# Optimization experiments

Hardware: AMD Instinct MI355X
Metric: run time of the kernel (lower is better)

The kernel has to match this reference:

```python
import jax, jax.numpy as jnp
import numpy as np

DIM = 96
HID = 384
DEPTH = 5
HEADS = 8
INNER = 64 * DIM          # inner_dim = dim_head * dim per source (dim_head=64)
DH = INNER // HEADS       # per-head dim = 768
SCALE = 64 ** -0.5        # scale uses default dim_head=64, not actual per-head dim
EPS = 1e-5


def setup_inputs() -> dict:
    key = jax.random.key(0)
    ks = jax.random.split(key, 13)
    def p(k, shape, s=0.02):
        return jax.random.normal(k, shape, jnp.float32) * s
    return {
        "x": jax.random.normal(ks[0], (2, 512, DIM), jnp.float32),
        "gam_a": p(ks[1], (DEPTH, 3, DIM)),          # attention pre-norm gammas
        "Wq": p(ks[2], (DEPTH, 3, DIM, INNER)),
        "Wk": p(ks[3], (DEPTH, 3, DIM, INNER)),
        "Wv": p(ks[4], (DEPTH, 3, DIM, INNER)),
        "Wo": p(ks[5], (DEPTH, 3, INNER, DIM)),
        "gam_m": p(ks[6], (DEPTH, 2, DIM)),          # MLP pre-norm gammas
        "W1": p(ks[7], (DEPTH, 2, DIM, HID)),
        "b1": p(ks[8], (DEPTH, 2, HID)),
        "W2": p(ks[9], (DEPTH, 2, HID, DIM)),
        "b2": p(ks[10], (DEPTH, 2, DIM)),
        "gam_mid": p(ks[11], (DEPTH, DIM)),          # bare LayerNorm inside each block
        "gam_final": p(ks[12], (DIM,)),
    }


def _ln(x, g):
    # nn.LayerNorm(elementwise_affine=False) followed by x * (gamma + 1)
    mu = x.mean(-1, keepdims=True)
    var = ((x - mu) ** 2).mean(-1, keepdims=True)
    return (x - mu) * jax.lax.rsqrt(var + EPS) * (g + 1.0)


def _attn(x, g, wq, wk, wv, wo):
    b, n, _ = x.shape
    h = _ln(x, g)                                    # self.norm (reuse_attention=True)
    q = (h @ wq).reshape(b, n, HEADS, DH).transpose(0, 2, 1, 3) * SCALE
    k = (h @ wk).reshape(b, n, HEADS, DH).transpose(0, 2, 1, 3)
    v = (h @ wv).reshape(b, n, HEADS, DH).transpose(0, 2, 1, 3)
    sim = jnp.einsum("bhid,bhjd->bhij", q, k)        # [b,h,n,n]
    a = jax.nn.softmax(sim, axis=-1)                 # dropout=0.0 -> identity
    o = jnp.einsum("bhij,bhjd->bhid", a, v)
    return o.transpose(0, 2, 1, 3).reshape(b, n, INNER) @ wo


def _mlp(x, g, w1, b1_, w2, b2_):
    # LayerNorm -> Linear -> GELU(exact) -> Linear (dropouts eval-mode identity)
    h = jax.nn.gelu(_ln(x, g) @ w1 + b1_, approximate=False)
    return h @ w2 + b2_


def reference(x, gam_a, Wq, Wk, Wv, Wo, gam_m, W1, b1, W2, b2, gam_mid, gam_final):
    for d in range(DEPTH):
        x = _attn(x, gam_a[d, 0], Wq[d, 0], Wk[d, 0], Wv[d, 0], Wo[d, 0]) + x
        x = _mlp(x, gam_m[d, 0], W1[d, 0], b1[d, 0], W2[d, 0], b2[d, 0]) + x
        x = _attn(x, gam_a[d, 1], Wq[d, 1], Wk[d, 1], Wv[d, 1], Wo[d, 1]) + x
        x = _attn(x, gam_a[d, 2], Wq[d, 2], Wk[d, 2], Wv[d, 2], Wo[d, 2]) + x
        x = _ln(x, gam_mid[d])                       # bare LayerNorm, NO residual
        x = _mlp(x, gam_m[d, 1], W1[d, 1], b1[d, 1], W2[d, 1], b2[d, 1]) + x
    return _ln(x, gam_final)
```

## Files before the change

### kernel.cpp

```cpp
#include <hip/hip_runtime.h>
#include <hip/hip_bf16.h>

typedef __hip_bfloat16 bf16;
typedef __attribute__((ext_vector_type(8))) short bf16x8;
typedef __attribute__((ext_vector_type(4))) float f32x4;

#define TOK    1024
#define DIM    96
#define HIDN   384
#define HEADS  8
#define DH     768
#define INNER  6144
#define SEQ    512
#define NDEPTH 5
#define EPSLN  1e-5f
#define QSCALE 0.125f

#define MFMA16(a, b, c) __builtin_amdgcn_mfma_f32_16x16x32_bf16((a), (b), (c), 0, 0, 0)

__device__ __forceinline__ float b2f(bf16 v) { return __bfloat162float(v); }
__device__ __forceinline__ bf16  f2b(float v) { return __float2bfloat16(v); }

__device__ __forceinline__ float gload(const void* p, size_t i, int f) {
  return f ? b2f(((const bf16*)p)[i]) : ((const float*)p)[i];
}
__device__ __forceinline__ const char* gptr(const void* base, size_t off, int f) {
  return (const char*)base + off * (size_t)(f ? 2 : 4);
}

__device__ __forceinline__ uint4 pack8(float4 u0, float4 u1) {
  alignas(16) unsigned short o[8];
  bf16 t;
  t = f2b(u0.x); o[0] = *(unsigned short*)&t;
  t = f2b(u0.y); o[1] = *(unsigned short*)&t;
  t = f2b(u0.z); o[2] = *(unsigned short*)&t;
  t = f2b(u0.w); o[3] = *(unsigned short*)&t;
  t = f2b(u1.x); o[4] = *(unsigned short*)&t;
  t = f2b(u1.y); o[5] = *(unsigned short*)&t;
  t = f2b(u1.z); o[6] = *(unsigned short*)&t;
  t = f2b(u1.w); o[7] = *(unsigned short*)&t;
  return *(const uint4*)o;
}

__global__ __launch_bounds__(256) void detect_kernel(const void* xraw, int* flag) {
  __shared__ int cnt[256];
  int t = threadIdx.x;
  const unsigned short* u = (const unsigned short*)xraw;
  int c = 0;
  #pragma unroll
  for (int i = 0; i < 4; i++) {
    unsigned short h = u[2 * (t * 4 + i)];
    int e = (h >> 7) & 0xFF;
    if (e >= 87 && e <= 132) c++;
  }
  cnt[t] = c;
  __syncthreads();
  for (int s = 128; s > 0; s >>= 1) {
    if (t < s) cnt[t] += cnt[t + s];
    __syncthreads();
  }
  if (t == 0) *flag = (cnt[0] > 700) ? 1 : 0;
}

__global__ __launch_bounds__(256) void wtrans_all_kernel(
    const void* __restrict__ Wo, const void* __restrict__ W1,
    const void* __restrict__ W2, bf16* __restrict__ woT,
    bf16* __restrict__ w1T, bf16* __restrict__ w2T,
    const int* __restrict__ flagp) {
  __shared__ float tile[32][65];
  int f = *flagp;
  int b = blockIdx.x;
  const void* src; bf16* dst; int R, C, bx, by, bz;
  if (b < 5760) {
    src = Wo; dst = woT; R = INNER; C = DIM;
    bz = b / 384; int rem = b % 384; bx = rem & 1; by = rem >> 1;
  } else if (b < 5940) {
    int idx = b - 5760;
    src = W1; dst = w1T; R = DIM; C = HIDN;
    bx = idx % 6; by = (idx / 6) % 3; bz = idx / 18;
  } else {
    int idx = b - 5940;
    src = W2; dst = w2T; R = HIDN; C = DIM;
    bx = idx & 1; by = (idx >> 1) % 12; bz = idx / 24;
  }
  int t = threadIdx.x;
  int c0 = bx * 64, r0 = by * 32;
  size_t bb = (size_t)bz * R * C;
  int ty = t >> 4, tx = t & 15;
  #pragma unroll
  for (int half = 0; half < 2; half++) {
    int r = r0 + ty + half * 16;
    int c = c0 + tx * 4;
    if (c < C) {
      size_t idx = bb + (size_t)r * C + c;
      float v0, v1, v2, v3;
      if (f) {
        uint2 u = *(const uint2*)((const unsigned short*)src + idx);
        v0 = __uint_as_float((u.x & 0xffffu) << 16);
        v1 = __uint_as_float(u.x & 0xffff0000u);
        v2 = __uint_as_float((u.y & 0xffffu) << 16);
        v3 = __uint_as_float(u.y & 0xffff0000u);
      } else {
        float4 v = *(const float4*)((const float*)src + idx);
        v0 = v.x; v1 = v.y; v2 = v.z; v3 = v.w;
      }
      tile[ty + half * 16][tx * 4 + 0] = v0;
      tile[ty + half * 16][tx * 4 + 1] = v1;
      tile[ty + half * 16][tx * 4 + 2] = v2;
      tile[ty + half * 16][tx * 4 + 3] = v3;
    }
  }
  __syncthreads();
  int cc = c0 + (t >> 2), rseg = (t & 3) * 8;
  if (cc < C) {
    int cs = cc - c0;
    alignas(16) unsigned short o[8];
    #pragma unroll
    for (int j = 0; j < 8; j++) {
      bf16 tv = f2b(tile[rseg + j][cs]);
      o[j] = *(unsigned short*)&tv;
    }
    *(uint4*)&dst[bb + (size_t)cc * R + r0 + rseg] = *(const uint4*)o;
  }
}

template <int WM>
__device__ __forceinline__ void gemm_bt_body(
    const void* __restrict__ A, int aF32, int lda,
    const void* __restrict__ Bt, int bF32, int ldb,
    int m0, int n0, int kbeg, int kend, int Mtot, int N,
    float alpha, bf16* __restrict__ Cb, float* __restrict__ Cf, int ldc) {
  constexpr int TM = WM * 32;
  __shared__ bf16 As[TM][40];
  __shared__ bf16 Bs[128][40];
  int t = threadIdx.x;
  int lane = t & 63;
  int wave = t >> 6;
  int wm = (wave >> 1) * (WM * 16), wn = (wave & 1) * 64;
  f32x4 acc[WM][4];
  #pragma unroll
  for (int i = 0; i < WM; i++)
    #pragma unroll
    for (int j = 0; j < 4; j++) acc[i][j] = (f32x4){0.f, 0.f, 0.f, 0.f};

  int arow = t >> 2, aseg = (t & 3) * 8;

  for (int kb = kbeg; kb < kend; kb += 32) {
    #pragma unroll
    for (int i = 0; i < (TM + 63) / 64; i++) {
      int rr = arow + i * 64;
      if ((TM % 64 == 0) || rr < TM) {
        int gm = min(m0 + rr, Mtot - 1);
        size_t idx = (size_t)gm * lda + kb + aseg;
        if (aF32) {
          const float* Af = (const float*)A;
          float4 u0 = *(const float4*)(Af + idx);
          float4 u1 = *(const float4*)(Af + idx + 4);
          *(uint4*)&As[rr][aseg] = pack8(u0, u1);
        } else {
          *(uint4*)&As[rr][aseg] = *(const uint4*)((const bf16*)A + idx);
        }
      }
    }
    #pragma unroll
    for (int i = 0; i < 2; i++) {
      int r = arow + i * 64;
      int gn = n0 + r;
      if (gn < N) {
        size_t idx = (size_t)gn * ldb + kb + aseg;
        if (bF32) {
          const float* Bf = (const float*)Bt;
          float4 u0 = *(const float4*)(Bf + idx);
          float4 u1 = *(const float4*)(Bf + idx + 4);
          *(uint4*)&Bs[r][aseg] = pack8(u0, u1);
        } else {
          *(uint4*)&Bs[r][aseg] = *(const uint4*)((const bf16*)Bt + idx);
        }
      } else {
        uint4 zz = {0, 0, 0, 0};
        *(uint4*)&Bs[r][aseg] = zz;
      }
    }
    __syncthreads();
    int fm = lane & 15, fq = (lane >> 4) * 8;
    bf16x8 af[WM], bfv[4];
    #pragma unroll
    for (int i = 0; i < WM; i++)
      af[i] = *(const bf16x8*)&As[wm + i * 16 + fm][fq];
    #pragma unroll
    for (int j = 0; j < 4; j++)
      bfv[j] = *(const bf16x8*)&Bs[wn + j * 16 + fm][fq];
    #pragma unroll
    for (int i = 0; i < WM; i++)
      #pragma unroll
      for (int j = 0; j < 4; j++)
        acc[i][j] = MFMA16(af[i], bfv[j], acc[i][j]);
    __syncthreads();
  }
  int col = lane & 15, rq = (lane >> 4) * 4;
  #pragma unroll
  for (int j = 0; j < 4; j++) {
    int gn = n0 + wn + j * 16 + col;
    if (gn >= N) continue;
    #pragma unroll
    for (int i = 0; i < WM; i++) {
      #pragma unroll
      for (int r = 0; r < 4; r++) {
        int gm = m0 + wm + i * 16 + rq + r;
        if (gm >= Mtot) continue;
        if (Cf) Cf[(size_t)gm * ldc + gn] = acc[i][j][r];
        else    Cb[(size_t)gm * ldc + gn] = f2b(acc[i][j][r] * alpha);
      }
    }
  }
}

__global__ __launch_bounds__(256) void mtgt_kernel(
    const void* __restrict__ WqE, const void* __restrict__ WkE,
    const void* __restrict__ WvE, const bf16* __restrict__ woT,
    float* __restrict__ P, const int* __restrict__ flagp) {
  int f = *flagp;
  int z = blockIdx.z;
  int ks = blockIdx.x / 3, mt = blockIdx.x % 3;
  bool isM = z < 120;
  int zz = isM ? z : z - 120;
  int L = zz >> 3, h = zz & 7;
  size_t wo = (size_t)L * DIM * INNER + (size_t)h * DH;
  const void* A  = isM ? (const void*)((const char*)WkE + wo * (f ? 2 : 4))
                       : (const void*)(woT + wo);
  const void* Bt = isM ? (const void*)((const char*)WqE + wo * (f ? 2 : 4))
                       : (const void*)((const char*)WvE + wo * (f ? 2 : 4));
  int aF32 = isM ? !f : 0;
  int bF32 = !f;
  float* Cf = P + ((size_t)ks * 240 + z) * DIM * DIM;
  gemm_bt_body<1>(A, aF32, INNER, Bt, bF32, INNER,
                  mt * 32, 0, ks * (DH / 2), (ks + 1) * (DH / 2), DIM, DIM,
                  1.f, nullptr, Cf, DIM);
}

__device__ __forceinline__ void ln_row_vals(float v0, float v1in, int lane,
    const char* g, int f, float& o0, float& o1) {
  float v1 = (lane < 32) ? v1in : 0.f;
  float s = v0 + v1;
  #pragma unroll
  for (int off = 32; off > 0; off >>= 1) s += __shfl_xor(s, off);
  float mu = s * (1.f / 96.f);
  float d0 = v0 - mu;
  float d1 = (lane < 32) ? (v1 - mu) : 0.f;
  float q = d0 * d0 + d1 * d1;
  #pragma unroll
  for (int off = 32; off > 0; off >>= 1) q += __shfl_xor(q, off);
  float rstd = rsqrtf(q * (1.f / 96.f) + EPSLN);
  o0 = d0 * rstd * (gload(g, lane, f) + 1.f);
  o1 = (lane < 32) ? (d1 * rstd * (gload(g, 64 + lane, f) + 1.f)) : 0.f;
}

__device__ __forceinline__ void store_hn(bf16* hn, bf16* hnT, int row, int lane,
                                         float o0, float o1) {
  size_t base = (size_t)row * DIM;
  bf16* hT = hnT + (size_t)(row >> 9) * DIM * SEQ;
  int ss = row & (SEQ - 1);
  hn[base + lane] = f2b(o0);
  hT[(size_t)lane * SEQ + ss] = f2b(o0);
  if (lane < 32) {
    hn[base + 64 + lane] = f2b(o1);
    hT[(size_t)(64 + lane) * SEQ + ss] = f2b(o1);
  }
}

__global__ __launch_bounds__(256) void cvtcast_kernel(
    const float* __restrict__ P, bf16* __restrict__ Mt, bf16* __restrict__ Gt,
    const void* __restrict__ in_x, float* __restrict__ x,
    bf16* __restrict__ hn, bf16* __restrict__ hnT,
    const void* __restrict__ gb, const int* __restrict__ flagp) {
  if (blockIdx.x < 2160) {
    const int n = 240 * DIM * DIM;
    int i0 = (blockIdx.x * 256 + threadIdx.x) * 4;
    if (i0 >= n) return;
    int z = i0 / (DIM * DIM);
    bool isM = z < 120;
    float alpha = isM ? QSCALE : 1.f;
    float4 a = *(const float4*)(P + i0);
    float4 b = *(const float4*)(P + n + i0);
    bf16* out = isM ? (Mt + i0) : (Gt + (size_t)i0 - (size_t)120 * DIM * DIM);
    alignas(8) unsigned short o[4];
    bf16 t;
    t = f2b((a.x + b.x) * alpha); o[0] = *(unsigned short*)&t;
    t = f2b((a.y + b.y) * alpha); o[1] = *(unsigned short*)&t;
    t = f2b((a.z + b.z) * alpha); o[2] = *(unsigned short*)&t;
    t = f2b((a.w + b.w) * alpha); o[3] = *(unsigned short*)&t;
    *(uint2*)out = *(const uint2*)o;
  } else {
    int f = *flagp;
    int wave = threadIdx.x >> 6, lane = threadIdx.x & 63;
    int row = (blockIdx.x - 2160) * 4 + wave;
    size_t base = (size_t)row * DIM;
    float v0 = gload(in_x, base + lane, f);
    float v1 = (lane < 32) ? gload(in_x, base + 64 + lane, f) : 0.f;
    x[base + lane] = v0;
    if (lane < 32) x[base + 64 + lane] = v1;
    float o0, o1;
    ln_row_vals(v0, v1, lane, gptr(gb, 0, f), f, o0, o1);
    store_hn(hn, hnT, row, lane, o0, o1);
  }
}

__global__ __launch_bounds__(256) void ln_kernel(
    const float* __restrict__ x, bf16* __restrict__ hn, bf16* __restrict__ hnT,
    const void* __restrict__ gb, size_t goff, const int* __restrict__ flagp) {
  int f = *flagp;
  int wave = threadIdx.x >> 6, lane = threadIdx.x & 63;
  int row = blockIdx.x * 4 + wave;
  size_t base = (size_t)row * DIM;
  float v0 = x[base + lane];
  float v1 = (lane < 32) ? x[base + 64 + lane] : 0.f;
  float o0, o1;
  ln_row_vals(v0, v1, lane, gptr(gb, goff, f), f, o0, o1);
  store_hn(hn, hnT, row, lane, o0, o1);
}

__global__ __launch_bounds__(512) void fattn5_kernel(
    const bf16* __restrict__ hn,
    const bf16* __restrict__ hnT,
    const bf16* __restrict__ MtL,
    const bf16* __restrict__ GtL,
    float* __restrict__ x) {
  __shared__ bf16 tP[16][520];
  __shared__ bf16 Zs[16][104];
  __shared__ float red[2][8][16];
  int tid = threadIdx.x, lane = tid & 63, wave = tid >> 6;
  int fm = lane & 15, fq = (lane >> 4) * 8;
  int col = lane & 15, rq = (lane >> 4) * 4;
  int z = blockIdx.y, b = z >> 3, h = z & 7;
  int m0 = blockIdx.x * 16;
  const bf16* hnB = hn + (size_t)b * SEQ * DIM;
  const bf16* hTB = hnT + (size_t)b * DIM * SEQ;
  const bf16* MtH = MtL + (size_t)h * DIM * DIM;
  const bf16* GtH = GtL + (size_t)h * DIM * DIM;

  if (wave < 6) {
    int n = wave;
    f32x4 a0 = (f32x4){0.f, 0.f, 0.f, 0.f};
    #pragma unroll
    for (int kb = 0; kb < 96; kb += 32) {
      bf16x8 af = *(const bf16x8*)(hnB + (size_t)(m0 + fm) * DIM + kb + fq);
      bf16x8 bv = *(const bf16x8*)(MtH + (size_t)(n * 16 + fm) * DIM + kb + fq);
      a0 = MFMA16(af, bv, a0);
    }
    #pragma unroll
    for (int r = 0; r < 4; r++)
      Zs[rq + r][n * 16 + col] = f2b(a0[r]);
  }
  __syncthreads();

  f32x4 acc2[4];
  #pragma unroll
  for (int j = 0; j < 4; j++) acc2[j] = (f32x4){0.f, 0.f, 0.f, 0.f};
  #pragma unroll
  for (int kb = 0; kb < 96; kb += 32) {
    bf16x8 af = *(const bf16x8*)&Zs[fm][kb + fq];
    bf16x8 bv[4];
    #pragma unroll
    for (int j = 0; j < 4; j++)
      bv[j] = *(const bf16x8*)(hnB + (size_t)(wave * 64 + j * 16 + fm) * DIM + kb + fq);
    #pragma unroll
    for (int j = 0; j < 4; j++)
      acc2[j] = MFMA16(af, bv[j], acc2[j]);
  }

  float rmax[4];
  #pragma unroll
  for (int r = 0; r < 4; r++) {
    float m = -1e30f;
    #pragma unroll
    for (int j = 0; j < 4; j++) m = fmaxf(m, acc2[j][r]);
    rmax[r] = m;
  }
  #pragma unroll
  for (int s = 1; s < 16; s <<= 1)
    #pragma unroll
    for (int r = 0; r < 4; r++)
      rmax[r] = fmaxf(rmax[r], __shfl_xor(rmax[r], s));
  if (col == 0)
    #pragma unroll
    for (int r = 0; r < 4; r++) red[0][wave][rq + r] = rmax[r];
  __syncthreads();
  float rsum[4];
  #pragma unroll
  for (int r = 0; r < 4; r++) {
    int row = rq + r;
    float gm = red[0][0][row];
    #pragma unroll
    for (int q = 1; q < 8; q++) gm = fmaxf(gm, red[0][q][row]);
    float s = 0.f;
    #pragma unroll
    for (int j = 0; j < 4; j++) {
      float e = __expf(acc2[j][r] - gm);
      acc2[j][r] = e;
      s += e;
    }
    rsum[r] = s;
  }
  #pragma unroll
  for (int s = 1; s < 16; s <<= 1)
    #pragma unroll
    for (int r = 0; r < 4; r++)
      rsum[r] += __shfl_xor(rsum[r], s);
  if (col == 0)
    #pragma unroll
    for (int r = 0; r < 4; r++) red[1][wave][rq + r] = rsum[r];
  __syncthreads();

  #pragma unroll
  for (int r = 0; r < 4; r++) {
    int row = rq + r;
    float tot = red[1][0][row];
    #pragma unroll
    for (int q = 1; q < 8; q++) tot += red[1][q][row];
    float inv = 1.f / tot;
    #pragma unroll
    for (int j = 0; j < 4; j++)
      tP[row][wave * 64 + j * 16 + col] = f2b(acc2[j][r] * inv);
  }
  __syncthreads();

  if (wave < 6) {
    int n = wave;
    f32x4 z0 = (f32x4){0.f, 0.f, 0.f, 0.f};
    #pragma unroll 4
    for (int kb = 0; kb < 512; kb += 32) {
      bf16x8 bv = *(const bf16x8*)(hTB + (size_t)(n * 16 + fm) * SEQ + kb + fq);
      bf16x8 af = *(const bf16x8*)&tP[fm][kb + fq];
      z0 = MFMA16(af, bv, z0);
    }
    __syncthreads();
    #pragma unroll
    for (int r = 0; r < 4; r++)
      Zs[rq + r][n * 16 + col] = f2b(z0[r]);
  } else {
    __syncthreads();
  }
  __syncthreads();

  if (wave < 6) {
    int n = wave;
    f32x4 o0 = (f32x4){0.f, 0.f, 0.f, 0.f};
    #pragma unroll
    for (int kb = 0; kb < 96; kb += 32) {
      bf16x8 af = *(const bf16x8*)&Zs[fm][kb + fq];
      bf16x8 bv = *(const bf16x8*)(GtH + (size_t)(n * 16 + fm) * DIM + kb + fq);
      o0 = MFMA16(af, bv, o0);
    }
    #pragma unroll
    for (int r = 0; r < 4; r++) {
      int gr = b * SEQ + m0 + rq + r;
      atomicAdd(x + (size_t)gr * DIM + n * 16 + col, o0[r]);
    }
  }
}

__global__ __launch_bounds__(512) void fmlp_kernel(
    float* __restrict__ X,
    const void* __restrict__ gmidb, size_t gmidoff, int useMid,
    const void* __restrict__ gmb, size_t gmoff,
    const bf16* __restrict__ w1T,
    const void* __restrict__ b1b, size_t b1off,
    const bf16* __restrict__ w2T,
    const void* __restrict__ b2b, size_t b2off,
    int lnmode, const void* __restrict__ lngb, size_t lngoff,
    bf16* __restrict__ hn, bf16* __restrict__ hnT, void* __restrict__ dout,
    const int* __restrict__ flagp) {
  __shared__ float X1s[32][96];
  __shared__ bf16 As[32][104];
  __shared__ bf16 Hs[32][392];
  int f = *flagp;
  int tid = threadIdx.x, lane = tid & 63, wave = tid >> 6;
  int fm = lane & 15, fq = (lane >> 4) * 8;
  int col = lane & 15, rq = (lane >> 4) * 4;
  int m0 = blockIdx.x * 32;
  const char* gm = gptr(gmb, gmoff, f);
  float gm0 = gload(gm, lane, f) + 1.f;
  float gm1 = (lane < 32) ? (gload(gm, 64 + lane, f) + 1.f) : 0.f;
  float gd0 = 1.f, gd1 = 1.f;
  if (useMid) {
    const char* gmid = gptr(gmidb, gmidoff, f);
    gd0 = gload(gmid, lane, f) + 1.f;
    gd1 = (lane < 32) ? (gload(gmid, 64 + lane, f) + 1.f) : 0.f;
  }
  for (int r = wave; r < 32; r += 8) {
    const float* xr = X + (size_t)(m0 + r) * DIM;
    float v0 = xr[lane];
    float v1 = (lane < 32) ? xr[64 + lane] : 0.f;
    if (useMid) {
      float s = v0 + v1;
      #pragma unroll
      for (int off = 32; off > 0; off >>= 1) s += __shfl_xor(s, off);
      float mu = s * (1.f / 96.f);
      float d0 = v0 - mu;
      float d1 = (lane < 32) ? (v1 - mu) : 0.f;
      float q = d0 * d0 + d1 * d1;
      #pragma unroll
      for (int off = 32; off > 0; off >>= 1) q += __shfl_xor(q, off);
      float rstd = rsqrtf(q * (1.f / 96.f) + EPSLN);
      v0 = d0 * rstd * gd0;
      v1 = (lane < 32) ? (d1 * rstd * gd1) : 0.f;
    }
    X1s[r][lane] = v0;
    if (lane < 32) X1s[r][64 + lane] = v1;
    float s = v0 + v1;
    #pragma unroll
    for (int off = 32; off > 0; off >>= 1) s += __shfl_xor(s, off);
    float mu = s * (1.f / 96.f);
    float d0 = v0 - mu;
    float d1 = (lane < 32) ? (v1 - mu) : 0.f;
    float q = d0 * d0 + d1 * d1;
    #pragma unroll
    for (int off = 32; off > 0; off >>= 1) q += __shfl_xor(q, off);
    float rstd = rsqrtf(q * (1.f / 96.f) + EPSLN);
    As[r][lane] = f2b(d0 * rstd * gm0);
    if (lane < 32) As[r][64 + lane] = f2b(d1 * rstd * gm1);
  }
  __syncthreads();

  int mw = wave & 1, nh = wave >> 1;
  f32x4 acc1[6];
  #pragma unroll
  for (int j = 0; j < 6; j++) acc1[j] = (f32x4){0.f, 0.f, 0.f, 0.f};
  #pragma unroll
  for (int kb = 0; kb < 96; kb += 32) {
    bf16x8 af = *(const bf16x8*)&As[mw * 16 + fm][kb + fq];
    #pragma unroll
    for (int j = 0; j < 6; j++) {
      bf16x8 bv = *(const bf16x8*)(w1T + (size_t)(nh * 96 + j * 16 + fm) * DIM + kb + fq);
      acc1[j] = MFMA16(af, bv, acc1[j]);
    }
  }
  const char* b1p = gptr(b1b, b1off, f);
  #pragma unroll
  for (int j = 0; j < 6; j++) {
    int gn = nh * 96 + j * 16 + col;
    float bv = gload(b1p, gn, f);
    #pragma unroll
    for (int r = 0; r < 4; r++) {
      float v = acc1[j][r] + bv;
      v = 0.5f * v * (1.f + erff(v * 0.70710678118f));
      Hs[mw * 16 + rq + r][gn] = f2b(v);
    }
  }
  __syncthreads();

  if (wave < 6) {
    int mA = wave & 1, nb = wave >> 1;
    f32x4 o0 = (f32x4){0.f, 0.f, 0.f, 0.f}, o1 = o0;
    #pragma unroll 4
    for (int kb = 0; kb < 384; kb += 32) {
      bf16x8 af = *(const bf16x8*)&Hs[mA * 16 + fm][kb + fq];
      bf16x8 b0 = *(const bf16x8*)(w2T + (size_t)(nb * 16 + fm) * HIDN + kb + fq);
      bf16x8 b1 = *(const bf16x8*)(w2T + (size_t)((nb + 3) * 16 + fm) * HIDN + kb + fq);
      o0 = MFMA16(af, b0, o0);
      o1 = MFMA16(af, b1, o1);
    }
    const char* b2p = gptr(b2b, b2off, f);
    float bb0 = gload(b2p, nb * 16 + col, f);
    float bb1 = gload(b2p, (nb + 3) * 16 + col, f);
    #pragma unroll
    for (int r = 0; r < 4; r++) {
      int row = mA * 16 + rq + r;
      int gmr = m0 + row;
      float nv0 = X1s[row][nb * 16 + col] + o0[r] + bb0;
      float nv1 = X1s[row][(nb + 3) * 16 + col] + o1[r] + bb1;
      X[(size_t)gmr * DIM + nb * 16 + col] = nv0;
      X[(size_t)gmr * DIM + (nb + 3) * 16 + col] = nv1;
      X1s[row][nb * 16 + col] = nv0;
      X1s[row][(nb + 3) * 16 + col] = nv1;
    }
  }
  __syncthreads();

  const char* lg = gptr(lngb, lngoff, f);
  for (int r = wave; r < 32; r += 8) {
    int row = m0 + r;
    size_t base = (size_t)row * DIM;
    float v0 = X1s[r][lane];
    float v1 = (lane < 32) ? X1s[r][64 + lane] : 0.f;
    float o0, o1;
    ln_row_vals(v0, v1, lane, lg, f, o0, o1);
    if (lnmode == 1) {
      store_hn(hn, hnT, row, lane, o0, o1);
    } else {
      if (!f) {
        ((float*)dout)[base + lane] = o0;
        if (lane < 32) ((float*)dout)[base + 64 + lane] = o1;
      } else {
        ((bf16*)dout)[base + lane] = f2b(o0);
        if (lane < 32) ((bf16*)dout)[base + 64 + lane] = f2b(o1);
      }
    }
  }
}

extern "C" void kernel_launch(void* const* d_in, const int* in_sizes, int n_in,
                              void* d_out, int out_size, void* d_ws, size_t ws_size,
                              hipStream_t stream) {
  const void* in_x    = d_in[0];
  const void* gam_a   = d_in[1];
  const void* Wq      = d_in[2];
  const void* Wk      = d_in[3];
  const void* Wv      = d_in[4];
  const void* Wo      = d_in[5];
  const void* gam_m   = d_in[6];
  const void* W1      = d_in[7];
  const void* b1      = d_in[8];
  const void* W2      = d_in[9];
  const void* b2      = d_in[10];
  const void* gam_mid = d_in[11];
  const void* gam_fin = d_in[12];

  char* wsb = (char*)d_ws;
  size_t off = 0;
  auto carve = [&](size_t bytes) {
    char* p = wsb + off;
    off += (bytes + 255) & ~(size_t)255;
    return p;
  };
  int*   flag = (int*)carve(256);
  float* x    = (float*)carve((size_t)TOK * DIM * 4);
  bf16*  hn   = (bf16*)carve((size_t)TOK * DIM * 2);
  bf16*  hnT  = (bf16*)carve((size_t)2 * DIM * SEQ * 2);
  const size_t WSZ = (size_t)15 * DIM * INNER;
  bf16*  woT  = (bf16*)carve(WSZ * 2);
  bf16*  w1T  = (bf16*)carve((size_t)10 * DIM * HIDN * 2);
  bf16*  w2T  = (bf16*)carve((size_t)10 * DIM * HIDN * 2);
  bf16*  Mt   = (bf16*)carve((size_t)120 * DIM * DIM * 2);
  bf16*  Gt   = (bf16*)carve((size_t)120 * DIM * DIM * 2);
  float* MtP  = (float*)carve((size_t)2 * 240 * DIM * DIM * 4);

  detect_kernel<<<dim3(1), dim3(256), 0, stream>>>(in_x, flag);

  wtrans_all_kernel<<<dim3(6180), dim3(256), 0, stream>>>(
      Wo, W1, W2, woT, w1T, w2T, flag);
  mtgt_kernel<<<dim3(6, 1, 240), dim3(256), 0, stream>>>(
      Wq, Wk, Wv, woT, MtP, flag);
  cvtcast_kernel<<<dim3(2160 + 256), dim3(256), 0, stream>>>(
      MtP, Mt, Gt, in_x, x, hn, hnT, gam_a, flag);

  auto attn = [&](int d, int j) {
    size_t gi = ((size_t)d * 3 + j);
    fattn5_kernel<<<dim3(32, 16), dim3(512), 0, stream>>>(
        hn, hnT, Mt + gi * 8 * DIM * DIM, Gt + gi * 8 * DIM * DIM, x);
  };

  for (int d = 0; d < NDEPTH; d++) {
    bool last = (d == NDEPTH - 1);
    attn(d, 0);
    fmlp_kernel<<<dim3(32), dim3(512), 0, stream>>>(
        x, nullptr, 0, 0,
        gam_m, (size_t)(d * 2 + 0) * DIM,
        w1T + (size_t)(d * 2 + 0) * DIM * HIDN, b1, (size_t)(d * 2 + 0) * HIDN,
        w2T + (size_t)(d * 2 + 0) * DIM * HIDN, b2, (size_t)(d * 2 + 0) * DIM,
        1, gam_a, (size_t)(d * 3 + 1) * DIM, hn, hnT, nullptr, flag);
    attn(d, 1);
    ln_kernel<<<dim3(TOK / 4), dim3(256), 0, stream>>>(
        x, hn, hnT, gam_a, (size_t)(d * 3 + 2) * DIM, flag);
    attn(d, 2);
    fmlp_kernel<<<dim3(32), dim3(512), 0, stream>>>(
        x, gam_mid, (size_t)d * DIM, 1,
        gam_m, (size_t)(d * 2 + 1) * DIM,
        w1T + (size_t)(d * 2 + 1) * DIM * HIDN, b1, (size_t)(d * 2 + 1) * HIDN,
        w2T + (size_t)(d * 2 + 1) * DIM * HIDN, b2, (size_t)(d * 2 + 1) * DIM,
        last ? 2 : 1, last ? gam_fin : gam_a,
        last ? (size_t)0 : (size_t)((d + 1) * 3) * DIM,
        hn, hnT, d_out, flag);
  }
}
```

Measured before the change: 646.8 us.

## Merge weight-prep kernels into staged launches and halve MLP row tile

The weight transposes and the Wk·Wq product GEMMs now share one launch. The Wo·Wv products and the Mt conversion share a second launch, and the Gt conversion plus input LayerNorm share a third. This removes launch serialization and fills the GPU better during preprocessing. Separately, the fused MLP kernel now processes 16 rows per block instead of 32 and launches 64 blocks, so more CUs are busy. In exchange, each block reuses its weight loads across fewer rows.

```diff
diff --git a/kernel.cpp b/kernel.cpp
--- a/kernel.cpp
+++ b/kernel.cpp
@@ -15,6 +15,8 @@
 #define NDEPTH 5
 #define EPSLN  1e-5f
 #define QSCALE 0.125f
+#define NMT    (120 * DIM * DIM)
+#define NP     (240 * DIM * DIM)
 
 #define MFMA16(a, b, c) __builtin_amdgcn_mfma_f32_16x16x32_bf16((a), (b), (c), 0, 0, 0)
 
@@ -62,27 +64,10 @@
   if (t == 0) *flag = (cnt[0] > 700) ? 1 : 0;
 }
 
-__global__ __launch_bounds__(256) void wtrans_all_kernel(
-    const void* __restrict__ Wo, const void* __restrict__ W1,
-    const void* __restrict__ W2, bf16* __restrict__ woT,
-    bf16* __restrict__ w1T, bf16* __restrict__ w2T,
-    const int* __restrict__ flagp) {
+__device__ void wtrans_body(const void* __restrict__ src, int R, int C,
+                            bf16* __restrict__ dst, int bx, int by, int bz,
+                            int f) {
   __shared__ float tile[32][65];
-  int f = *flagp;
-  int b = blockIdx.x;
-  const void* src; bf16* dst; int R, C, bx, by, bz;
-  if (b < 5760) {
-    src = Wo; dst = woT; R = INNER; C = DIM;
-    bz = b / 384; int rem = b % 384; bx = rem & 1; by = rem >> 1;
-  } else if (b < 5940) {
-    int idx = b - 5760;
-    src = W1; dst = w1T; R = DIM; C = HIDN;
-    bx = idx % 6; by = (idx / 6) % 3; bz = idx / 18;
-  } else {
-    int idx = b - 5940;
-    src = W2; dst = w2T; R = HIDN; C = DIM;
-    bx = idx & 1; by = (idx >> 1) % 12; bz = idx / 24;
-  }
   int t = threadIdx.x;
   int c0 = bx * 64, r0 = by * 32;
   size_t bb = (size_t)bz * R * C;
@@ -124,50 +109,40 @@
   }
 }
 
-template <int WM>
-__device__ __forceinline__ void gemm_bt_body(
+__device__ void gemm_bt32_body(
     const void* __restrict__ A, int aF32, int lda,
     const void* __restrict__ Bt, int bF32, int ldb,
-    int m0, int n0, int kbeg, int kend, int Mtot, int N,
-    float alpha, bf16* __restrict__ Cb, float* __restrict__ Cf, int ldc) {
-  constexpr int TM = WM * 32;
-  __shared__ bf16 As[TM][40];
+    int m0, int kbeg, int kend, int N,
+    float* __restrict__ Cf, int ldc) {
+  __shared__ bf16 As[32][40];
   __shared__ bf16 Bs[128][40];
   int t = threadIdx.x;
   int lane = t & 63;
   int wave = t >> 6;
-  int wm = (wave >> 1) * (WM * 16), wn = (wave & 1) * 64;
-  f32x4 acc[WM][4];
-  #pragma unroll
-  for (int i = 0; i < WM; i++)
-    #pragma unroll
-    for (int j = 0; j < 4; j++) acc[i][j] = (f32x4){0.f, 0.f, 0.f, 0.f};
+  int wm = (wave >> 1) * 16, wn = (wave & 1) * 64;
+  f32x4 acc[4];
+  #pragma unroll
+  for (int j = 0; j < 4; j++) acc[j] = (f32x4){0.f, 0.f, 0.f, 0.f};
 
   int arow = t >> 2, aseg = (t & 3) * 8;
 
   for (int kb = kbeg; kb < kend; kb += 32) {
-    #pragma unroll
-    for (int i = 0; i < (TM + 63) / 64; i++) {
-      int rr = arow + i * 64;
-      if ((TM % 64 == 0) || rr < TM) {
-        int gm = min(m0 + rr, Mtot - 1);
-        size_t idx = (size_t)gm * lda + kb + aseg;
-        if (aF32) {
-          const float* Af = (const float*)A;
-          float4 u0 = *(const float4*)(Af + idx);
-          float4 u1 = *(const float4*)(Af + idx + 4);
-          *(uint4*)&As[rr][aseg] = pack8(u0, u1);
-        } else {
-          *(uint4*)&As[rr][aseg] = *(const uint4*)((const bf16*)A + idx);
-        }
+    if (arow < 32) {
+      size_t idx = (size_t)(m0 + arow) * lda + kb + aseg;
+      if (aF32) {
+        const float* Af = (const float*)A;
+        float4 u0 = *(const float4*)(Af + idx);
+        float4 u1 = *(const float4*)(Af + idx + 4);
+        *(uint4*)&As[arow][aseg] = pack8(u0, u1);
+      } else {
+        *(uint4*)&As[arow][aseg] = *(const uint4*)((const bf16*)A + idx);
       }
     }
     #pragma unroll
     for (int i = 0; i < 2; i++) {
       int r = arow + i * 64;
-      int gn = n0 + r;
-      if (gn < N) {
-        size_t idx = (size_t)gn * ldb + kb + aseg;
+      if (r < N) {
+        size_t idx = (size_t)r * ldb + kb + aseg;
         if (bF32) {
           const float* Bf = (const float*)Bt;
           float4 u0 = *(const float4*)(Bf + idx);
@@ -183,47 +158,37 @@
     }
     __syncthreads();
     int fm = lane & 15, fq = (lane >> 4) * 8;
-    bf16x8 af[WM], bfv[4];
-    #pragma unroll
-    for (int i = 0; i < WM; i++)
-      af[i] = *(const bf16x8*)&As[wm + i * 16 + fm][fq];
+    bf16x8 af = *(const bf16x8*)&As[wm + fm][fq];
+    bf16x8 bfv[4];
     #pragma unroll
     for (int j = 0; j < 4; j++)
       bfv[j] = *(const bf16x8*)&Bs[wn + j * 16 + fm][fq];
     #pragma unroll
-    for (int i = 0; i < WM; i++)
-      #pragma unroll
-      for (int j = 0; j < 4; j++)
-        acc[i][j] = MFMA16(af[i], bfv[j], acc[i][j]);
+    for (int j = 0; j < 4; j++)
+      acc[j] = MFMA16(af, bfv[j], acc[j]);
     __syncthreads();
   }
   int col = lane & 15, rq = (lane >> 4) * 4;
   #pragma unroll
   for (int j = 0; j < 4; j++) {
-    int gn = n0 + wn + j * 16 + col;
+    int gn = wn + j * 16 + col;
     if (gn >= N) continue;
     #pragma unroll
-    for (int i = 0; i < WM; i++) {
-      #pragma unroll
-      for (int r = 0; r < 4; r++) {
-        int gm = m0 + wm + i * 16 + rq + r;
-        if (gm >= Mtot) continue;
-        if (Cf) Cf[(size_t)gm * ldc + gn] = acc[i][j][r];
-        else    Cb[(size_t)gm * ldc + gn] = f2b(acc[i][j][r] * alpha);
-      }
-    }
-  }
-}
-
-__global__ __launch_bounds__(256) void mtgt_kernel(
+    for (int r = 0; r < 4; r++) {
+      int gm = m0 + wm + rq + r;
+      Cf[(size_t)gm * ldc + gn] = acc[j][r];
+    }
+  }
+}
+
+__device__ void mtgt_body(int idx, int isM,
     const void* __restrict__ WqE, const void* __restrict__ WkE,
     const void* __restrict__ WvE, const bf16* __restrict__ woT,
-    float* __restrict__ P, const int* __restrict__ flagp) {
-  int f = *flagp;
-  int z = blockIdx.z;
-  int ks = blockIdx.x / 3, mt = blockIdx.x % 3;
-  bool isM = z < 120;
-  int zz = isM ? z : z - 120;
+    float* __restrict__ P, int f) {
+  int zz = idx / 6;
+  int rem = idx % 6;
+  int ks = rem / 3, mt = rem % 3;
+  int z = isM ? zz : (120 + zz);
   int L = zz >> 3, h = zz & 7;
   size_t wo = (size_t)L * DIM * INNER + (size_t)h * DH;
   const void* A  = isM ? (const void*)((const char*)WkE + wo * (f ? 2 : 4))
@@ -233,9 +198,21 @@
   int aF32 = isM ? !f : 0;
   int bF32 = !f;
   float* Cf = P + ((size_t)ks * 240 + z) * DIM * DIM;
-  gemm_bt_body<1>(A, aF32, INNER, Bt, bF32, INNER,
-                  mt * 32, 0, ks * (DH / 2), (ks + 1) * (DH / 2), DIM, DIM,
-                  1.f, nullptr, Cf, DIM);
+  gemm_bt32_body(A, aF32, INNER, Bt, bF32, INNER,
+                 mt * 32, ks * (DH / 2), (ks + 1) * (DH / 2), DIM, Cf, DIM);
+}
+
+__device__ __forceinline__ void cvt4(const float* __restrict__ P, size_t i0,
+                                     float alpha, bf16* __restrict__ out) {
+  float4 a = *(const float4*)(P + i0);
+  float4 b = *(const float4*)(P + (size_t)NP + i0);
+  alignas(8) unsigned short o[4];
+  bf16 t;
+  t = f2b((a.x + b.x) * alpha); o[0] = *(unsigned short*)&t;
+  t = f2b((a.y + b.y) * alpha); o[1] = *(unsigned short*)&t;
+  t = f2b((a.z + b.z) * alpha); o[2] = *(unsigned short*)&t;
+  t = f2b((a.w + b.w) * alpha); o[3] = *(unsigned short*)&t;
+  *(uint2*)out = *(const uint2*)o;
 }
 
 __device__ __forceinline__ void ln_row_vals(float v0, float v1in, int lane,
@@ -268,32 +245,55 @@
   }
 }
 
-__global__ __launch_bounds__(256) void cvtcast_kernel(
-    const float* __restrict__ P, bf16* __restrict__ Mt, bf16* __restrict__ Gt,
+__global__ __launch_bounds__(256) void prep1_kernel(
+    const void* __restrict__ Wo, const void* __restrict__ W1,
+    const void* __restrict__ W2, bf16* __restrict__ woT,
+    bf16* __restrict__ w1T, bf16* __restrict__ w2T,
+    const void* __restrict__ WqE, const void* __restrict__ WkE,
+    float* __restrict__ P, const int* __restrict__ flagp) {
+  int f = *flagp;
+  int b = blockIdx.x;
+  if (b < 5760) {
+    int bz = b / 384; int rem = b % 384;
+    wtrans_body(Wo, INNER, DIM, woT, rem & 1, rem >> 1, bz, f);
+  } else if (b < 5940) {
+    int idx = b - 5760;
+    wtrans_body(W1, DIM, HIDN, w1T, idx % 6, (idx / 6) % 3, idx / 18, f);
+  } else if (b < 6180) {
+    int idx = b - 5940;
+    wtrans_body(W2, HIDN, DIM, w2T, idx & 1, (idx >> 1) % 12, idx / 24, f);
+  } else {
+    mtgt_body(b - 6180, 1, WqE, WkE, nullptr, nullptr, P, f);
+  }
+}
+
+__global__ __launch_bounds__(256) void prep2_kernel(
+    const void* __restrict__ WvE, const bf16* __restrict__ woT,
+    float* __restrict__ P, bf16* __restrict__ Mt,
+    const int* __restrict__ flagp) {
+  int f = *flagp;
+  int b = blockIdx.x;
+  if (b < 720) {
+    mtgt_body(b, 0, nullptr, nullptr, WvE, woT, P, f);
+  } else {
+    size_t i0 = ((size_t)(b - 720) * 256 + threadIdx.x) * 4;
+    if (i0 < (size_t)NMT) cvt4(P, i0, QSCALE, Mt + i0);
+  }
+}
+
+__global__ __launch_bounds__(256) void prep3_kernel(
+    const float* __restrict__ P, bf16* __restrict__ Gt,
     const void* __restrict__ in_x, float* __restrict__ x,
     bf16* __restrict__ hn, bf16* __restrict__ hnT,
     const void* __restrict__ gb, const int* __restrict__ flagp) {
-  if (blockIdx.x < 2160) {
-    const int n = 240 * DIM * DIM;
-    int i0 = (blockIdx.x * 256 + threadIdx.x) * 4;
-    if (i0 >= n) return;
-    int z = i0 / (DIM * DIM);
-    bool isM = z < 120;
-    float alpha = isM ? QSCALE : 1.f;
-    float4 a = *(const float4*)(P + i0);
-    float4 b = *(const float4*)(P + n + i0);
-    bf16* out = isM ? (Mt + i0) : (Gt + (size_t)i0 - (size_t)120 * DIM * DIM);
-    alignas(8) unsigned short o[4];
-    bf16 t;
-    t = f2b((a.x + b.x) * alpha); o[0] = *(unsigned short*)&t;
-    t = f2b((a.y + b.y) * alpha); o[1] = *(unsigned short*)&t;
-    t = f2b((a.z + b.z) * alpha); o[2] = *(unsigned short*)&t;
-    t = f2b((a.w + b.w) * alpha); o[3] = *(unsigned short*)&t;
-    *(uint2*)out = *(const uint2*)o;
+  int b = blockIdx.x;
+  if (b < 1080) {
+    size_t loc = ((size_t)b * 256 + threadIdx.x) * 4;
+    if (loc < (size_t)NMT) cvt4(P, (size_t)NMT + loc, 1.f, Gt + loc);
   } else {
     int f = *flagp;
     int wave = threadIdx.x >> 6, lane = threadIdx.x & 63;
-    int row = (blockIdx.x - 2160) * 4 + wave;
+    int row = (b - 1080) * 4 + wave;
     size_t base = (size_t)row * DIM;
     float v0 = gload(in_x, base + lane, f);
     float v1 = (lane < 32) ? gload(in_x, base + 64 + lane, f) : 0.f;
@@ -470,14 +470,14 @@
     int lnmode, const void* __restrict__ lngb, size_t lngoff,
     bf16* __restrict__ hn, bf16* __restrict__ hnT, void* __restrict__ dout,
     const int* __restrict__ flagp) {
-  __shared__ float X1s[32][96];
-  __shared__ bf16 As[32][104];
-  __shared__ bf16 Hs[32][392];
+  __shared__ float X1s[16][96];
+  __shared__ bf16 As[16][104];
+  __shared__ bf16 Hs[16][392];
   int f = *flagp;
   int tid = threadIdx.x, lane = tid & 63, wave = tid >> 6;
   int fm = lane & 15, fq = (lane >> 4) * 8;
   int col = lane & 15, rq = (lane >> 4) * 4;
-  int m0 = blockIdx.x * 32;
+  int m0 = blockIdx.x * 16;
   const char* gm = gptr(gmb, gmoff, f);
   float gm0 = gload(gm, lane, f) + 1.f;
   float gm1 = (lane < 32) ? (gload(gm, 64 + lane, f) + 1.f) : 0.f;
@@ -487,7 +487,7 @@
     gd0 = gload(gmid, lane, f) + 1.f;
     gd1 = (lane < 32) ? (gload(gmid, 64 + lane, f) + 1.f) : 0.f;
   }
-  for (int r = wave; r < 32; r += 8) {
+  for (int r = wave; r < 16; r += 8) {
     const float* xr = X + (size_t)(m0 + r) * DIM;
     float v0 = xr[lane];
     float v1 = (lane < 32) ? xr[64 + lane] : 0.f;
@@ -522,63 +522,56 @@
   }
   __syncthreads();
 
-  int mw = wave & 1, nh = wave >> 1;
-  f32x4 acc1[6];
-  #pragma unroll
-  for (int j = 0; j < 6; j++) acc1[j] = (f32x4){0.f, 0.f, 0.f, 0.f};
+  f32x4 acc1[3];
+  #pragma unroll
+  for (int j = 0; j < 3; j++) acc1[j] = (f32x4){0.f, 0.f, 0.f, 0.f};
   #pragma unroll
   for (int kb = 0; kb < 96; kb += 32) {
-    bf16x8 af = *(const bf16x8*)&As[mw * 16 + fm][kb + fq];
-    #pragma unroll
-    for (int j = 0; j < 6; j++) {
-      bf16x8 bv = *(const bf16x8*)(w1T + (size_t)(nh * 96 + j * 16 + fm) * DIM + kb + fq);
+    bf16x8 af = *(const bf16x8*)&As[fm][kb + fq];
+    #pragma unroll
+    for (int j = 0; j < 3; j++) {
+      bf16x8 bv = *(const bf16x8*)(w1T + (size_t)((wave * 3 + j) * 16 + fm) * DIM + kb + fq);
       acc1[j] = MFMA16(af, bv, acc1[j]);
     }
   }
   const char* b1p = gptr(b1b, b1off, f);
   #pragma unroll
-  for (int j = 0; j < 6; j++) {
-    int gn = nh * 96 + j * 16 + col;
+  for (int j = 0; j < 3; j++) {
+    int gn = (wave * 3 + j) * 16 + col;
     float bv = gload(b1p, gn, f);
     #pragma unroll
     for (int r = 0; r < 4; r++) {
       float v = acc1[j][r] + bv;
       v = 0.5f * v * (1.f + erff(v * 0.70710678118f));
-      Hs[mw * 16 + rq + r][gn] = f2b(v);
+      Hs[rq + r][gn] = f2b(v);
     }
   }
   __syncthreads();
 
   if (wave < 6) {
-    int mA = wave & 1, nb = wave >> 1;
-    f32x4 o0 = (f32x4){0.f, 0.f, 0.f, 0.f}, o1 = o0;
+    int n = wave;
+    f32x4 o0 = (f32x4){0.f, 0.f, 0.f, 0.f};
     #pragma unroll 4
     for (int kb = 0; kb < 384; kb += 32) {
-      bf16x8 af = *(const bf16x8*)&Hs[mA * 16 + fm][kb + fq];
-      bf16x8 b0 = *(const bf16x8*)(w2T + (size_t)(nb * 16 + fm) * HIDN + kb + fq);
-      bf16x8 b1 = *(const bf16x8*)(w2T + (size_t)((nb + 3) * 16 + fm) * HIDN + kb + fq);
-      o0 = MFMA16(af, b0, o0);
-      o1 = MFMA16(af, b1, o1);
+      bf16x8 af = *(const bf16x8*)&Hs[fm][kb + fq];
+      bf16x8 bv = *(const bf16x8*)(w2T + (size_t)(n * 16 + fm) * HIDN + kb + fq);
+      o0 = MFMA16(af, bv, o0);
     }
     const char* b2p = gptr(b2b, b2off, f);
-    float bb0 = gload(b2p, nb * 16 + col, f);
-    float bb1 = gload(b2p, (nb + 3) * 16 + col, f);
+    float bb0 = gload(b2p, n * 16 + col, f);
     #pragma unroll
     for (int r = 0; r < 4; r++) {
-      int row = mA * 16 + rq + r;
+      int row = rq + r;
       int gmr = m0 + row;
-      float nv0 = X1s[row][nb * 16 + col] + o0[r] + bb0;
-      float nv1 = X1s[row][(nb + 3) * 16 + col] + o1[r] + bb1;
-      X[(size_t)gmr * DIM + nb * 16 + col] = nv0;
-      X[(size_t)gmr * DIM + (nb + 3) * 16 + col] = nv1;
-      X1s[row][nb * 16 + col] = nv0;
-      X1s[row][(nb + 3) * 16 + col] = nv1;
+      float nv0 = X1s[row][n * 16 + col] + o0[r] + bb0;
+      X[(size_t)gmr * DIM + n * 16 + col] = nv0;
+      X1s[row][n * 16 + col] = nv0;
     }
   }
   __syncthreads();
 
   const char* lg = gptr(lngb, lngoff, f);
-  for (int r = wave; r < 32; r += 8) {
+  for (int r = wave; r < 16; r += 8) {
     int row = m0 + r;
     size_t base = (size_t)row * DIM;
     float v0 = X1s[r][lane];
@@ -631,18 +624,18 @@
   bf16*  woT  = (bf16*)carve(WSZ * 2);
   bf16*  w1T  = (bf16*)carve((size_t)10 * DIM * HIDN * 2);
   bf16*  w2T  = (bf16*)carve((size_t)10 * DIM * HIDN * 2);
-  bf16*  Mt   = (bf16*)carve((size_t)120 * DIM * DIM * 2);
-  bf16*  Gt   = (bf16*)carve((size_t)120 * DIM * DIM * 2);
-  float* MtP  = (float*)carve((size_t)2 * 240 * DIM * DIM * 4);
+  bf16*  Mt   = (bf16*)carve((size_t)NMT * 2);
+  bf16*  Gt   = (bf16*)carve((size_t)NMT * 2);
+  float* MtP  = (float*)carve((size_t)2 * NP * 4);
 
   detect_kernel<<<dim3(1), dim3(256), 0, stream>>>(in_x, flag);
 
-  wtrans_all_kernel<<<dim3(6180), dim3(256), 0, stream>>>(
-      Wo, W1, W2, woT, w1T, w2T, flag);
-  mtgt_kernel<<<dim3(6, 1, 240), dim3(256), 0, stream>>>(
-      Wq, Wk, Wv, woT, MtP, flag);
-  cvtcast_kernel<<<dim3(2160 + 256), dim3(256), 0, stream>>>(
-      MtP, Mt, Gt, in_x, x, hn, hnT, gam_a, flag);
+  prep1_kernel<<<dim3(6900), dim3(256), 0, stream>>>(
+      Wo, W1, W2, woT, w1T, w2T, Wq, Wk, MtP, flag);
+  prep2_kernel<<<dim3(1800), dim3(256), 0, stream>>>(
+      Wv, woT, MtP, Mt, flag);
+  prep3_kernel<<<dim3(1336), dim3(256), 0, stream>>>(
+      MtP, Gt, in_x, x, hn, hnT, gam_a, flag);
 
   auto attn = [&](int d, int j) {
     size_t gi = ((size_t)d * 3 + j);
@@ -653,7 +646,7 @@
   for (int d = 0; d < NDEPTH; d++) {
     bool last = (d == NDEPTH - 1);
     attn(d, 0);
-    fmlp_kernel<<<dim3(32), dim3(512), 0, stream>>>(
+    fmlp_kernel<<<dim3(64), dim3(512), 0, stream>>>(
         x, nullptr, 0, 0,
         gam_m, (size_t)(d * 2 + 0) * DIM,
         w1T + (size_t)(d * 2 + 0) * DIM * HIDN, b1, (size_t)(d * 2 + 0) * HIDN,
@@ -663,7 +656,7 @@
     ln_kernel<<<dim3(TOK / 4), dim3(256), 0, stream>>>(
         x, hn, hnT, gam_a, (size_t)(d * 3 + 2) * DIM, flag);
     attn(d, 2);
-    fmlp_kernel<<<dim3(32), dim3(512), 0, stream>>>(
+    fmlp_kernel<<<dim3(64), dim3(512), 0, stream>>>(
         x, gam_mid, (size_t)d * DIM, 1,
         gam_m, (size_t)(d * 2 + 1) * DIM,
         w1T + (size_t)(d * 2 + 1) * DIM * HIDN, b1, (size_t)(d * 2 + 1) * HIDN,
```

Result: faster. 581.8 us (-10.1%).
